# Kernel optimization log

Hardware: AMD Instinct MI355X
Metric: run time of the kernel (lower is better)

## Reference

```python
import jax, jax.numpy as jnp
import numpy as np

N_NODES = 100000
N_EDGES = 1600000
IN_F = 67
H1, C1 = 10, 8   # heads, per-head channels layer 1
H2, C2 = 1, 1    # layer 2


def setup_inputs() -> dict:
    key = jax.random.key(0)
    ks = jax.random.split(key, 10)
    x = jax.random.normal(ks[0], (N_NODES, IN_F), dtype=jnp.float32)
    edge_index = jax.random.randint(ks[1], (2, N_EDGES), 0, N_NODES, dtype=jnp.int64)
    s = 0.1
    W1 = jax.random.normal(ks[2], (IN_F, H1 * C1), dtype=jnp.float32) * s
    att_src1 = jax.random.normal(ks[3], (H1, C1), dtype=jnp.float32) * s
    att_dst1 = jax.random.normal(ks[4], (H1, C1), dtype=jnp.float32) * s
    b1 = jnp.zeros((H1 * C1,), dtype=jnp.float32)
    W2 = jax.random.normal(ks[5], (H1 * C1, H2 * C2), dtype=jnp.float32) * s
    att_src2 = jax.random.normal(ks[6], (H2, C2), dtype=jnp.float32) * s
    att_dst2 = jax.random.normal(ks[7], (H2, C2), dtype=jnp.float32) * s
    b2 = jnp.zeros((H2 * C2,), dtype=jnp.float32)
    return {"x": x, "edge_index": edge_index, "W1": W1, "att_src1": att_src1,
            "att_dst1": att_dst1, "b1": b1, "W2": W2, "att_src2": att_src2,
            "att_dst2": att_dst2, "b2": b2}


def gat_conv(x, src, dst, W, att_src, att_dst, bias, heads, out_ch):
    """PyG GATConv (eval mode): gather -> leaky_relu -> segment softmax -> scatter."""
    n = x.shape[0]
    h = (x @ W).reshape(n, heads, out_ch)                     # [N,H,C]
    a_src = jnp.sum(h * att_src, axis=-1)                     # [N,H]
    a_dst = jnp.sum(h * att_dst, axis=-1)                     # [N,H]
    e = a_src[src] + a_dst[dst]                               # [E,H]
    e = jax.nn.leaky_relu(e, negative_slope=0.2)
    # numerically stable softmax over edges grouped by destination node
    m = jax.ops.segment_max(e, dst, num_segments=n)           # [N,H]
    ex = jnp.exp(e - m[dst])
    denom = jax.ops.segment_sum(ex, dst, num_segments=n)      # [N,H]
    alpha = ex / denom[dst]                                   # [E,H]
    msg = h[src] * alpha[:, :, None]                          # [E,H,C]
    out = jax.ops.segment_sum(msg, dst, num_segments=n)       # [N,H,C]
    return out.reshape(n, heads * out_ch) + bias


def reference(x, edge_index, W1, att_src1, att_dst1, b1, W2, att_src2, att_dst2, b2):
    n = x.shape[0]
    loops = jnp.arange(n, dtype=edge_index.dtype)
    src = jnp.concatenate([edge_index[0], loops])             # add_self_loops=True
    dst = jnp.concatenate([edge_index[1], loops])
    h = gat_conv(x, src, dst, W1, att_src1, att_dst1, b1, H1, C1)
    h = jax.nn.elu(h)
    out = gat_conv(h, src, dst, W2, att_src2, att_dst2, b2, H2, C2)
    return out
```

## Files before the change

### kernel.cpp

```cpp
#include <hip/hip_runtime.h>
#include <math.h>

#define IN_F 67
#define F1   80
#define NH1  10
#define NC1  8

#define GN   64
#define KS   104
#define PKS  96

#define CB    512
#define CSH   9
#define NBC   196
#define RB    64
#define FPC   8
#define NGRP  8
#define GCAP  1536
#define SLCAP 1792
#define CSTRIDE 16
#define NFB   512
#define CHUNK 2048

typedef _Float16 h16;
typedef h16 h16x2 __attribute__((ext_vector_type(2)));
typedef h16 h16x8 __attribute__((ext_vector_type(8)));
typedef float f32x4 __attribute__((ext_vector_type(4)));
typedef float f32x4u __attribute__((ext_vector_type(4), aligned(4)));
typedef int i32x4 __attribute__((ext_vector_type(4)));

__global__ __launch_bounds__(256)
void k_front(const float* __restrict__ x, const float* __restrict__ W,
             const float* __restrict__ att_s, const float* __restrict__ att_d,
             const int* __restrict__ ei, int* __restrict__ gcur,
             int* __restrict__ ebuf, h16* __restrict__ pk,
             float* __restrict__ a_dst, int N, int E) {
    __shared__ __align__(16) char smem[GN * 81 * 4];
    const int tid = threadIdx.x;

    if ((int)blockIdx.x < NFB) {
        int2* sStage = (int2*)smem;
        int*  sCnt   = (int*)(smem + CHUNK * 8);
        int*  sGBase = sCnt + NBC;
        int*  sScan  = sGBase + NBC;
        const int g = blockIdx.x & (NGRP - 1);

        for (int base_e = blockIdx.x * CHUNK; base_e < E; base_e += NFB * CHUNK) {
            int lim = E - base_e; if (lim > CHUNK) lim = CHUNK;
            for (int i = tid; i < NBC; i += 256) sCnt[i] = 0;
            __syncthreads();

            int2 ev[8]; int pos[8]; int nloc = 0;
            int e0 = base_e + tid * 8;
            if (tid * 8 + 8 <= lim) {
                i32x4 s0 = *(const i32x4*)(ei + e0);
                i32x4 s1 = *(const i32x4*)(ei + e0 + 4);
                i32x4 d0 = *(const i32x4*)(ei + E + e0);
                i32x4 d1 = *(const i32x4*)(ei + E + e0 + 4);
#pragma unroll
                for (int j = 0; j < 4; ++j) { ev[j] = make_int2(s0[j], d0[j]); }
#pragma unroll
                for (int j = 0; j < 4; ++j) { ev[4 + j] = make_int2(s1[j], d1[j]); }
                nloc = 8;
            } else {
                for (int j = 0; j < 8; ++j) {
                    int e = e0 + j;
                    if (tid * 8 + j < lim) { ev[nloc++] = make_int2(ei[e], ei[E + e]); }
                }
            }
            for (int j = 0; j < nloc; ++j)
                pos[j] = atomicAdd(&sCnt[ev[j].y >> CSH], 1);
            __syncthreads();

            int v = (tid < NBC) ? sCnt[tid] : 0;
            sScan[tid] = v;
            __syncthreads();
            for (int o = 1; o < 256; o <<= 1) {
                int u = (tid >= o) ? sScan[tid - o] : 0;
                __syncthreads();
                sScan[tid] += u;
                __syncthreads();
            }
            for (int j = 0; j < nloc; ++j) {
                int B = ev[j].y >> CSH;
                sStage[sScan[B] - sCnt[B] + pos[j]] = ev[j];
            }
            if (tid < NBC && sCnt[tid] > 0)
                sGBase[tid] = atomicAdd(&gcur[((size_t)g * NBC + tid) * CSTRIDE], sCnt[tid]);
            __syncthreads();

            int total = sScan[NBC - 1];
            for (int i = tid; i < total; i += 256) {
                int2 e = sStage[i];
                int B = e.y >> CSH;
                int gp = sGBase[B] + (i - (sScan[B] - sCnt[B]));
                if (gp < GCAP)
                    ebuf[((size_t)g * NBC + B) * GCAP + gp] = e.x | ((e.y & (CB - 1)) << 17);
            }
            __syncthreads();
        }
        return;
    }

    h16*   sWt = (h16*)smem;
    float* sO  = (float*)smem;
    const int node0 = (blockIdx.x - NFB) * GN;

    if (tid < 240) {
        int c = tid - (tid >= 160 ? 160 : (tid >= 80 ? 80 : 0));
        int kb = (tid >= 160 ? 64 : (tid >= 80 ? 32 : 0));
        h16 tmp[32];
#pragma unroll
        for (int j = 0; j < 32; ++j) {
            int k = kb + j;
            tmp[j] = (h16)((k < IN_F) ? W[k * F1 + c] : 0.f);
        }
        h16* dst = sWt + c * KS + kb;
#pragma unroll
        for (int j = 0; j < 4; ++j)
            *(h16x8*)(dst + j * 8) = *(const h16x8*)(tmp + j * 8);
    }
    __syncthreads();

    const int lane = tid & 63;
    const int m    = lane & 15;
    const int quad = lane >> 4;
    const int wn0  = (tid >> 6) * 16;

    int gn  = node0 + wn0 + m;
    int gnc = gn < N ? gn : N - 1;
    const float* xr = x + (size_t)gnc * IN_F;

    f32x4 acc[5];
#pragma unroll
    for (int ct = 0; ct < 5; ++ct) acc[ct] = (f32x4){0.f, 0.f, 0.f, 0.f};

#pragma unroll
    for (int ks = 0; ks < 64; ks += 32) {
        int k0 = ks + quad * 8;
        f32x4 a0 = *(const f32x4u*)(xr + k0);
        f32x4 a1 = *(const f32x4u*)(xr + k0 + 4);
        h16x8 af;
        af[0] = (h16)a0.x; af[1] = (h16)a0.y; af[2] = (h16)a0.z; af[3] = (h16)a0.w;
        af[4] = (h16)a1.x; af[5] = (h16)a1.y; af[6] = (h16)a1.z; af[7] = (h16)a1.w;
#pragma unroll
        for (int ct = 0; ct < 5; ++ct) {
            h16x8 bf = *(const h16x8*)(sWt + (ct * 16 + m) * KS + ks + quad * 8);
            acc[ct] = __builtin_amdgcn_mfma_f32_16x16x32_f16(af, bf, acc[ct], 0, 0, 0);
        }
    }
    {
        h16x8 af = (h16x8)(h16)0.f;
        if (quad == 0) {
            af[0] = (h16)xr[64]; af[1] = (h16)xr[65]; af[2] = (h16)xr[66];
        }
#pragma unroll
        for (int ct = 0; ct < 5; ++ct) {
            h16x8 bf = *(const h16x8*)(sWt + (ct * 16 + m) * KS + 64 + quad * 8);
            acc[ct] = __builtin_amdgcn_mfma_f32_16x16x32_f16(af, bf, acc[ct], 0, 0, 0);
        }
    }
    __syncthreads();

#pragma unroll
    for (int ct = 0; ct < 5; ++ct)
#pragma unroll
        for (int r = 0; r < 4; ++r)
            sO[(wn0 + quad * 4 + r) * 81 + ct * 16 + m] = acc[ct][r];
    __syncthreads();

    for (int idx = tid; idx < GN * (F1 / 2); idx += 256) {
        int n = idx / (F1 / 2);
        int p = idx - n * (F1 / 2);
        int gg = node0 + n;
        if (gg < N) {
            h16x2 v;
            v.x = (h16)sO[n * 81 + 2 * p];
            v.y = (h16)sO[n * 81 + 2 * p + 1];
            *(h16x2*)(pk + (size_t)gg * PKS + 2 * p) = v;
        }
    }
    for (int t = tid; t < GN * NH1; t += 256) {
        int n = t / NH1;
        int h = t - n * NH1;
        int gg = node0 + n;
        if (gg < N) {
            const float* hr = sO + n * 81 + h * NC1;
            float s = 0.f, d = 0.f;
#pragma unroll
            for (int c = 0; c < NC1; ++c) {
                float v = hr[c];
                s += v * att_s[h * NC1 + c];
                d += v * att_d[h * NC1 + c];
            }
            pk[(size_t)gg * PKS + F1 + h] = (h16)s;
            a_dst[gg * NH1 + h] = d;
        }
    }
}

__global__ __launch_bounds__(256)
void k_agg1(const int* __restrict__ ebuf, const int* __restrict__ gcur,
            const h16* __restrict__ pk, const float* __restrict__ a_dst,
            const float* __restrict__ b1, const float* __restrict__ W2,
            const float* __restrict__ att_s2, const float* __restrict__ att_d2,
            float2* __restrict__ hs2, float* __restrict__ a_dst2,
            int* __restrict__ row, int* __restrict__ deg, int* __restrict__ csr2,
            int N, int NB) {
    __shared__ int   sTmp[SLCAP];
    __shared__ int   sList[SLCAP];
    __shared__ int   s_cnt[RB];
    __shared__ int   s_scan[RB];
    __shared__ int   s_cur[RB];
    __shared__ float s_acc[RB];
    __shared__ int   sTot;

    const int tid = threadIdx.x;
    const int b = blockIdx.x;
    const int B = b >> 3;
    const int q = b & 7;
    const int lo = b * RB;

    for (int i = tid; i < RB; i += 256) { s_cnt[i] = 1; s_acc[i] = 0.f; }
    if (tid == 0) sTot = 0;
    __syncthreads();

    for (int g = 0; g < NGRP; ++g) {
        size_t slot = (size_t)g * NBC + B;
        int cnt = gcur[slot * CSTRIDE];
        cnt = cnt < GCAP ? cnt : GCAP;
        const int* eb = ebuf + slot * GCAP;
        for (int i = tid; i < cnt; i += 256) {
            int v = eb[i];
            int dloc = v >> 17;
            if ((dloc >> 6) == q) {
                int n_l = dloc & (RB - 1);
                atomicAdd(&s_cnt[n_l], 1);
                int p = atomicAdd(&sTot, 1);
                if (p < SLCAP) sTmp[p] = (v & 0x1FFFF) | (n_l << 17);
            }
        }
    }
    __syncthreads();

    if (tid < RB) s_scan[tid] = s_cnt[tid];
    __syncthreads();
    for (int o = 1; o < RB; o <<= 1) {
        int v = 0;
        if (tid < RB && tid >= o) v = s_scan[tid - o];
        __syncthreads();
        if (tid < RB) s_scan[tid] += v;
        __syncthreads();
    }
    if (tid < RB) {
        int excl = s_scan[tid] - s_cnt[tid];
        int n = lo + tid;
        if (excl < SLCAP) sList[excl] = n;
        s_cur[tid] = excl + 1;
        if (n < N) {
            int dg = s_cnt[tid];
            if (excl + dg > SLCAP) dg = SLCAP - excl > 0 ? SLCAP - excl : 0;
            row[n] = b * SLCAP + excl;
            deg[n] = dg;
        }
    }
    __syncthreads();

    int total = sTot < SLCAP ? sTot : SLCAP;
    for (int i = tid; i < total; i += 256) {
        int u = sTmp[i];
        int n_l = u >> 17;
        int p = atomicAdd(&s_cur[n_l], 1);
        if (p < SLCAP) sList[p] = u & 0x1FFFF;
    }
    __syncthreads();

    int tot2 = s_scan[RB - 1];
    tot2 = tot2 < SLCAP ? tot2 : SLCAP;
    for (int i = tid; i < tot2; i += 256)
        csr2[(size_t)b * SLCAP + i] = sList[i];

    for (int t = tid; t < RB * NH1; t += 256) {
        int n_l = t / NH1;
        int h = t - n_l * NH1;
        int n = lo + n_l;
        if (n >= N) continue;
        int beg = s_scan[n_l] - s_cnt[n_l];
        int end = beg + s_cnt[n_l];
        end = end < SLCAP ? end : SLCAP;
        float ad = a_dst[n * NH1 + h];
        float den = 0.f;
        float num[NC1];
#pragma unroll
        for (int c = 0; c < NC1; ++c) num[c] = 0.f;

        int i = beg;
        for (; i + 7 < end; i += 8) {
            int sv[8];
#pragma unroll
            for (int j = 0; j < 8; ++j) sv[j] = sList[i + j];
            h16x8 qf[8];
            float a[8];
#pragma unroll
            for (int j = 0; j < 8; ++j) {
                const h16* rp = pk + (size_t)sv[j] * PKS;
                qf[j] = *(const h16x8*)(rp + h * NC1);
                a[j] = (float)rp[F1 + h];
            }
#pragma unroll
            for (int j = 0; j < 8; ++j) {
                float v = a[j] + ad;
                v = v > 0.f ? v : 0.2f * v;
                float w = __expf(v);
                den += w;
#pragma unroll
                for (int c = 0; c < NC1; ++c) num[c] += w * (float)qf[j][c];
            }
        }
        for (; i + 3 < end; i += 4) {
            int sv[4];
#pragma unroll
            for (int j = 0; j < 4; ++j) sv[j] = sList[i + j];
            h16x8 qf[4];
            float a[4];
#pragma unroll
            for (int j = 0; j < 4; ++j) {
                const h16* rp = pk + (size_t)sv[j] * PKS;
                qf[j] = *(const h16x8*)(rp + h * NC1);
                a[j] = (float)rp[F1 + h];
            }
#pragma unroll
            for (int j = 0; j < 4; ++j) {
                float v = a[j] + ad;
                v = v > 0.f ? v : 0.2f * v;
                float w = __expf(v);
                den += w;
#pragma unroll
                for (int c = 0; c < NC1; ++c) num[c] += w * (float)qf[j][c];
            }
        }
        for (; i < end; ++i) {
            const h16* rp = pk + (size_t)sList[i] * PKS;
            h16x8 qf = *(const h16x8*)(rp + h * NC1);
            float v = (float)rp[F1 + h] + ad;
            v = v > 0.f ? v : 0.2f * v;
            float w = __expf(v);
            den += w;
#pragma unroll
            for (int c = 0; c < NC1; ++c) num[c] += w * (float)qf[c];
        }
        float inv = 1.f / den;
        const float* bb = b1 + h * NC1;
        const float* w2 = W2 + h * NC1;
        float p = 0.f;
#pragma unroll
        for (int c = 0; c < NC1; ++c) {
            float o = num[c] * inv + bb[c];
            o = o > 0.f ? o : expm1f(o);
            p += o * w2[c];
        }
        atomicAdd(&s_acc[n_l], p);
    }
    __syncthreads();

    if (tid < RB) {
        int n = lo + tid;
        if (n < N) {
            float acc = s_acc[tid];
            float2 v;
            v.x = acc;
            v.y = acc * att_s2[0];
            hs2[n] = v;
            a_dst2[n] = acc * att_d2[0];
        }
    }
}

__global__ __launch_bounds__(256)
void k_agg2(const int* __restrict__ row, const int* __restrict__ deg,
            const int* __restrict__ csr2, const float2* __restrict__ hs2,
            const float* __restrict__ a_dst2, const float* __restrict__ b2,
            float* __restrict__ out, int N) {
    int n = blockIdx.x * blockDim.x + threadIdx.x;
    if (n >= N) return;
    float ad = a_dst2[n];
    float den = 0.f, num = 0.f;
    int beg = row[n];
    int end = beg + deg[n];
    int i = beg;
    for (; i + 7 < end; i += 8) {
        int sv[8];
#pragma unroll
        for (int j = 0; j < 8; ++j) sv[j] = csr2[i + j];
        float2 g[8];
#pragma unroll
        for (int j = 0; j < 8; ++j) g[j] = hs2[sv[j]];
#pragma unroll
        for (int j = 0; j < 8; ++j) {
            float v = g[j].y + ad;
            v = v > 0.f ? v : 0.2f * v;
            float w = __expf(v);
            den += w;
            num += w * g[j].x;
        }
    }
    for (; i < end; ++i) {
        float2 g = hs2[csr2[i]];
        float v = g.y + ad;
        v = v > 0.f ? v : 0.2f * v;
        float w = __expf(v);
        den += w;
        num += w * g.x;
    }
    out[n] = num / den + b2[0];
}

extern "C" void kernel_launch(void* const* d_in, const int* in_sizes, int n_in,
                              void* d_out, int out_size, void* d_ws, size_t ws_size,
                              hipStream_t stream) {
    const float* x        = (const float*)d_in[0];
    const int*   ei       = (const int*)d_in[1];
    const float* W1       = (const float*)d_in[2];
    const float* att_src1 = (const float*)d_in[3];
    const float* att_dst1 = (const float*)d_in[4];
    const float* b1       = (const float*)d_in[5];
    const float* W2       = (const float*)d_in[6];
    const float* att_src2 = (const float*)d_in[7];
    const float* att_dst2 = (const float*)d_in[8];
    const float* b2       = (const float*)d_in[9];
    float* out = (float*)d_out;

    const int N  = in_sizes[0] / IN_F;
    const int E  = in_sizes[1] / 2;
    const int NB = (N + RB - 1) / RB;

    float*  ws      = (float*)d_ws;
    h16*    pk      = (h16*)ws;
    float*  a_dst1  = ws + (size_t)N * (PKS / 2);
    float2* hs2     = (float2*)(a_dst1 + (size_t)N * NH1);
    float*  a_dst2  = (float*)(hs2 + N);
    int*    row     = (int*)(a_dst2 + N);
    int*    deg     = row + N;
    int*    gcur    = deg + N;
    int*    csr2    = gcur + (size_t)NGRP * NBC * CSTRIDE;
    int*    ebuf    = csr2 + (size_t)NB * SLCAP;

    const int B = 256;
    const int nbG = (N + GN - 1) / GN;

    hipMemsetAsync(gcur, 0, (size_t)NGRP * NBC * CSTRIDE * sizeof(int), stream);
    k_front<<<NFB + nbG, 256, 0, stream>>>(x, W1, att_src1, att_dst1, ei,
                                           gcur, ebuf, pk, a_dst1, N, E);

    k_agg1<<<NB, 256, 0, stream>>>(ebuf, gcur, pk, a_dst1, b1, W2,
                                   att_src2, att_dst2, hs2, a_dst2,
                                   row, deg, csr2, N, NB);

    k_agg2<<<(N + B - 1) / B, B, 0, stream>>>(row, deg, csr2, hs2, a_dst2, b2, out, N);
}
```

Baseline: 243.9 us.

## Bucket edges directly by 128-node destination block to remove agg1 filtering

The front binning now partitions edges into fine buckets of 128 destination nodes (784 buckets, each thread scanning four counters) instead of 512-node coarse buckets. Each aggregation block then reads only its own eight group slots and copies them contiguously, with no filtering of other blocks' edges and no global shared counter atomic. This removes the eightfold redundant reads of coarse buckets in k_agg1, but it adds more global atomics per chunk in k_front, larger per-block shared memory, and per-bucket capacity limits that are tighter relative to mean load.

```diff
diff --git a/kernel.cpp b/kernel.cpp
--- a/kernel.cpp
+++ b/kernel.cpp
@@ -10,14 +10,13 @@
 #define KS   104
 #define PKS  96
 
-#define CB    512
-#define CSH   9
-#define NBC   196
-#define RB    64
-#define FPC   8
+#define RB    128
+#define RSH   7
+#define NBF_P 784
 #define NGRP  8
-#define GCAP  1536
-#define SLCAP 1792
+#define BCAP  512
+#define SLCAP 3072
+#define SLT   3328
 #define CSTRIDE 16
 #define NFB   512
 #define CHUNK 2048
@@ -34,20 +33,21 @@
              const float* __restrict__ att_s, const float* __restrict__ att_d,
              const int* __restrict__ ei, int* __restrict__ gcur,
              int* __restrict__ ebuf, h16* __restrict__ pk,
-             float* __restrict__ a_dst, int N, int E) {
-    __shared__ __align__(16) char smem[GN * 81 * 4];
+             float* __restrict__ a_dst, int N, int E, int NBF) {
+    __shared__ __align__(16) char smem[CHUNK * 8 + NBF_P * 12 + 1024];
     const int tid = threadIdx.x;
 
     if ((int)blockIdx.x < NFB) {
         int2* sStage = (int2*)smem;
         int*  sCnt   = (int*)(smem + CHUNK * 8);
-        int*  sGBase = sCnt + NBC;
-        int*  sScan  = sGBase + NBC;
+        int*  sOff   = sCnt + NBF_P;
+        int*  sGBase = sOff + NBF_P;
+        int*  sScan  = sGBase + NBF_P;
         const int g = blockIdx.x & (NGRP - 1);
 
         for (int base_e = blockIdx.x * CHUNK; base_e < E; base_e += NFB * CHUNK) {
             int lim = E - base_e; if (lim > CHUNK) lim = CHUNK;
-            for (int i = tid; i < NBC; i += 256) sCnt[i] = 0;
+            for (int i = tid; i < NBF_P; i += 256) sCnt[i] = 0;
             __syncthreads();
 
             int2 ev[8]; int pos[8]; int nloc = 0;
@@ -69,11 +69,14 @@
                 }
             }
             for (int j = 0; j < nloc; ++j)
-                pos[j] = atomicAdd(&sCnt[ev[j].y >> CSH], 1);
-            __syncthreads();
-
-            int v = (tid < NBC) ? sCnt[tid] : 0;
-            sScan[tid] = v;
+                pos[j] = atomicAdd(&sCnt[ev[j].y >> RSH], 1);
+            __syncthreads();
+
+            int base4 = tid * 4;
+            int v4[4]; int s4 = 0;
+#pragma unroll
+            for (int j = 0; j < 4; ++j) { v4[j] = sCnt[base4 + j]; s4 += v4[j]; }
+            sScan[tid] = s4;
             __syncthreads();
             for (int o = 1; o < 256; o <<= 1) {
                 int u = (tid >= o) ? sScan[tid - o] : 0;
@@ -81,21 +84,26 @@
                 sScan[tid] += u;
                 __syncthreads();
             }
+            int excl = sScan[tid] - s4;
+#pragma unroll
+            for (int j = 0; j < 4; ++j) { sOff[base4 + j] = excl; excl += v4[j]; }
+            __syncthreads();
+
             for (int j = 0; j < nloc; ++j) {
-                int B = ev[j].y >> CSH;
-                sStage[sScan[B] - sCnt[B] + pos[j]] = ev[j];
-            }
-            if (tid < NBC && sCnt[tid] > 0)
-                sGBase[tid] = atomicAdd(&gcur[((size_t)g * NBC + tid) * CSTRIDE], sCnt[tid]);
-            __syncthreads();
-
-            int total = sScan[NBC - 1];
-            for (int i = tid; i < total; i += 256) {
+                int B = ev[j].y >> RSH;
+                sStage[sOff[B] + pos[j]] = ev[j];
+            }
+            for (int t = tid; t < NBF_P; t += 256)
+                if (sCnt[t] > 0)
+                    sGBase[t] = atomicAdd(&gcur[((size_t)g * NBF + t) * CSTRIDE], sCnt[t]);
+            __syncthreads();
+
+            for (int i = tid; i < lim; i += 256) {
                 int2 e = sStage[i];
-                int B = e.y >> CSH;
-                int gp = sGBase[B] + (i - (sScan[B] - sCnt[B]));
-                if (gp < GCAP)
-                    ebuf[((size_t)g * NBC + B) * GCAP + gp] = e.x | ((e.y & (CB - 1)) << 17);
+                int B = e.y >> RSH;
+                int gp = sGBase[B] + (i - sOff[B]);
+                if (gp < BCAP)
+                    ebuf[((size_t)g * NBF + B) * BCAP + gp] = e.x | ((e.y & (RB - 1)) << 17);
             }
             __syncthreads();
         }
@@ -206,41 +214,36 @@
             const float* __restrict__ att_s2, const float* __restrict__ att_d2,
             float2* __restrict__ hs2, float* __restrict__ a_dst2,
             int* __restrict__ row, int* __restrict__ deg, int* __restrict__ csr2,
-            int N, int NB) {
+            int N, int NBF) {
     __shared__ int   sTmp[SLCAP];
-    __shared__ int   sList[SLCAP];
+    __shared__ int   sList[SLT];
     __shared__ int   s_cnt[RB];
     __shared__ int   s_scan[RB];
     __shared__ int   s_cur[RB];
     __shared__ float s_acc[RB];
-    __shared__ int   sTot;
 
     const int tid = threadIdx.x;
     const int b = blockIdx.x;
-    const int B = b >> 3;
-    const int q = b & 7;
     const int lo = b * RB;
 
     for (int i = tid; i < RB; i += 256) { s_cnt[i] = 1; s_acc[i] = 0.f; }
-    if (tid == 0) sTot = 0;
-    __syncthreads();
-
+    __syncthreads();
+
+    int off = 0;
+#pragma unroll
     for (int g = 0; g < NGRP; ++g) {
-        size_t slot = (size_t)g * NBC + B;
+        size_t slot = (size_t)g * NBF + b;
         int cnt = gcur[slot * CSTRIDE];
-        cnt = cnt < GCAP ? cnt : GCAP;
-        const int* eb = ebuf + slot * GCAP;
-        for (int i = tid; i < cnt; i += 256) {
-            int v = eb[i];
-            int dloc = v >> 17;
-            if ((dloc >> 6) == q) {
-                int n_l = dloc & (RB - 1);
-                atomicAdd(&s_cnt[n_l], 1);
-                int p = atomicAdd(&sTot, 1);
-                if (p < SLCAP) sTmp[p] = (v & 0x1FFFF) | (n_l << 17);
-            }
-        }
-    }
+        cnt = cnt < BCAP ? cnt : BCAP;
+        if (off + cnt > SLCAP) cnt = SLCAP - off;
+        const int* eb = ebuf + slot * BCAP;
+        for (int i = tid; i < cnt; i += 256) sTmp[off + i] = eb[i];
+        off += cnt;
+    }
+    int total = off;
+    __syncthreads();
+    for (int i = tid; i < total; i += 256)
+        atomicAdd(&s_cnt[sTmp[i] >> 17], 1);
     __syncthreads();
 
     if (tid < RB) s_scan[tid] = s_cnt[tid];
@@ -255,30 +258,29 @@
     if (tid < RB) {
         int excl = s_scan[tid] - s_cnt[tid];
         int n = lo + tid;
-        if (excl < SLCAP) sList[excl] = n;
+        if (excl < SLT) sList[excl] = n;
         s_cur[tid] = excl + 1;
         if (n < N) {
             int dg = s_cnt[tid];
-            if (excl + dg > SLCAP) dg = SLCAP - excl > 0 ? SLCAP - excl : 0;
-            row[n] = b * SLCAP + excl;
+            if (excl + dg > SLT) dg = SLT - excl > 0 ? SLT - excl : 0;
+            row[n] = b * SLT + excl;
             deg[n] = dg;
         }
     }
     __syncthreads();
 
-    int total = sTot < SLCAP ? sTot : SLCAP;
     for (int i = tid; i < total; i += 256) {
         int u = sTmp[i];
         int n_l = u >> 17;
         int p = atomicAdd(&s_cur[n_l], 1);
-        if (p < SLCAP) sList[p] = u & 0x1FFFF;
+        if (p < SLT) sList[p] = u & 0x1FFFF;
     }
     __syncthreads();
 
     int tot2 = s_scan[RB - 1];
-    tot2 = tot2 < SLCAP ? tot2 : SLCAP;
+    tot2 = tot2 < SLT ? tot2 : SLT;
     for (int i = tid; i < tot2; i += 256)
-        csr2[(size_t)b * SLCAP + i] = sList[i];
+        csr2[(size_t)b * SLT + i] = sList[i];
 
     for (int t = tid; t < RB * NH1; t += 256) {
         int n_l = t / NH1;
@@ -287,7 +289,7 @@
         if (n >= N) continue;
         int beg = s_scan[n_l] - s_cnt[n_l];
         int end = beg + s_cnt[n_l];
-        end = end < SLCAP ? end : SLCAP;
+        end = end < SLT ? end : SLT;
         float ad = a_dst[n * NH1 + h];
         float den = 0.f;
         float num[NC1];
@@ -430,9 +432,9 @@
     const float* b2       = (const float*)d_in[9];
     float* out = (float*)d_out;
 
-    const int N  = in_sizes[0] / IN_F;
-    const int E  = in_sizes[1] / 2;
-    const int NB = (N + RB - 1) / RB;
+    const int N   = in_sizes[0] / IN_F;
+    const int E   = in_sizes[1] / 2;
+    const int NBF = (N + RB - 1) / RB;
 
     float*  ws      = (float*)d_ws;
     h16*    pk      = (h16*)ws;
@@ -442,19 +444,19 @@
     int*    row     = (int*)(a_dst2 + N);
     int*    deg     = row + N;
     int*    gcur    = deg + N;
-    int*    csr2    = gcur + (size_t)NGRP * NBC * CSTRIDE;
-    int*    ebuf    = csr2 + (size_t)NB * SLCAP;
+    int*    csr2    = gcur + (size_t)NGRP * NBF * CSTRIDE;
+    int*    ebuf    = csr2 + (size_t)NBF * SLT;
 
     const int B = 256;
     const int nbG = (N + GN - 1) / GN;
 
-    hipMemsetAsync(gcur, 0, (size_t)NGRP * NBC * CSTRIDE * sizeof(int), stream);
+    hipMemsetAsync(gcur, 0, (size_t)NGRP * NBF * CSTRIDE * sizeof(int), stream);
     k_front<<<NFB + nbG, 256, 0, stream>>>(x, W1, att_src1, att_dst1, ei,
-                                           gcur, ebuf, pk, a_dst1, N, E);
-
-    k_agg1<<<NB, 256, 0, stream>>>(ebuf, gcur, pk, a_dst1, b1, W2,
-                                   att_src2, att_dst2, hs2, a_dst2,
-                                   row, deg, csr2, N, NB);
+                                           gcur, ebuf, pk, a_dst1, N, E, NBF);
+
+    k_agg1<<<NBF, 256, 0, stream>>>(ebuf, gcur, pk, a_dst1, b1, W2,
+                                    att_src2, att_dst2, hs2, a_dst2,
+                                    row, deg, csr2, N, NBF);
 
     k_agg2<<<(N + B - 1) / B, B, 0, stream>>>(row, deg, csr2, hs2, a_dst2, b2, out, N);
 }
```

Result: faster. 222.2 us (-8.9%).
